# Kernel tuning notes

Measured on AMD Instinct MI355X. Metric: run time of the kernel, lower is better.

Reference implementation:

```python
import jax, jax.numpy as jnp
import numpy as np

S, P, T, E, H = 32, 48, 8, 64, 64      # scenes, peds/scene, obs_len, embedding_dim, h_dim
D1, D2 = 512, 1024                      # mlp_pre_pool hidden / bottleneck dims
B = S * P
TOTAL_LEN = 20                          # obs_len + pred_len (8 + 12)


def setup_inputs() -> dict:
    key = jax.random.key(0)
    ks = jax.random.split(key, 10)
    h_states = jax.random.normal(ks[0], (1, B, H), jnp.float32)
    end_pos = jax.random.normal(ks[1], (B, 2), jnp.float32)
    traj = jax.random.normal(ks[2], (TOTAL_LEN, B, 2), jnp.float32)
    traj_weight = jax.random.uniform(ks[3], (S, P * P, 2, T), jnp.float32)
    starts = jnp.arange(S, dtype=jnp.int32) * P
    seq_start_end = jnp.stack([starts, starts + P], axis=1)  # uniform scenes of P peds
    # learned params
    W_se = jax.random.normal(ks[4], (T * E, 2 * T), jnp.float32) * 0.05  # spatial_embedding
    b_se = jnp.zeros((T * E,), jnp.float32)
    W1 = jax.random.normal(ks[5], (D1, T * E + H), jnp.float32) * 0.05   # 576 -> 512
    b1 = jnp.zeros((D1,), jnp.float32)
    W2 = jax.random.normal(ks[6], (D2, D1), jnp.float32) * 0.05          # 512 -> 1024
    b2 = jnp.zeros((D2,), jnp.float32)
    return {"h_states": h_states, "seq_start_end": seq_start_end, "end_pos": end_pos,
            "traj": traj, "traj_weight": traj_weight, "mlp_pre_pool_dim_0": T * E,
            "W_se": W_se, "b_se": b_se, "W1": W1, "b1": b1, "W2": W2, "b2": b2}


def reference(h_states, seq_start_end, end_pos, traj, traj_weight, mlp_pre_pool_dim_0,
              W_se, b_se, W1, b1, W2, b2):
    # obs_traj: (obs_len, B, 2) -> (B, T, 2) -> per-scene (S, P, T, 2)
    obs = traj[:T].transpose(1, 0, 2).reshape(S, P, T, 2)
    h = h_states.reshape(S, P, H)
    # pairwise history differences: row (i, j) = obs[j] - obs[i]  (gather-diff)
    rel = obs[:, None, :, :, :] - obs[:, :, None, :, :]          # (S, i, j, T, 2)
    rel = rel.reshape(S, P, P, 2 * T)                            # flatten (T,2) -> 2T
    emb = rel @ W_se.T + b_se                                    # (S, P, P, T*E)
    # traj_weight[i]: (P*P, 2, T) -> permute(0,2,1) -> tile channel to E -> flatten
    w = jnp.transpose(traj_weight, (0, 1, 3, 2))                 # (S, P*P, T, 2)
    w = jnp.tile(w, (1, 1, 1, E // 2)).reshape(S, P, P, T * E)
    emb = w * emb
    # curr_hidden_1: hidden of ped j broadcast over i
    hj = jnp.broadcast_to(h[:, None, :, :], (S, P, P, H))
    x = jnp.concatenate([emb, hj], axis=-1)                      # (S, P, P, 576)
    x = jax.nn.relu(x @ W1.T + b1)                               # (S, P, P, 512)
    x = jax.nn.relu(x @ W2.T + b2)                               # (S, P, P, 1024)
    pool_h = x.max(axis=2)                                       # max over j
    return pool_h.reshape(S * P, D2)
```

## Files before the change

kernel.cpp:

```cpp
#include <hip/hip_runtime.h>
#include <hip/hip_bf16.h>
#include <stdint.h>

#define S_  32
#define P_  48
#define T_  8
#define E_  64
#define H_  64
#define D1_ 512
#define D2_ 1024
#define B_  (S_*P_)
#define M_  (S_*P_*P_)
#define K1_ 576
#define KE_ 512

typedef __attribute__((ext_vector_type(8))) short  short8;
typedef __attribute__((ext_vector_type(8))) __bf16 bf16x8;
typedef __attribute__((ext_vector_type(4))) float  f32x4;
typedef __attribute__((ext_vector_type(8))) float  f32x8;

__device__ inline short f2bf(float x) {
  union { float f; unsigned u; } v; v.f = x;
  unsigned r = v.u + 0x7FFFu + ((v.u >> 16) & 1u);
  return (short)(r >> 16);
}

__device__ inline void async16(const void* g, void* l) {
  __builtin_amdgcn_global_load_lds(
      (const __attribute__((address_space(1))) void*)g,
      (__attribute__((address_space(3))) void*)l, 16, 0, 0);
}

__device__ inline f32x4 mfma16(short8 a, short8 b, f32x4 c) {
  return __builtin_amdgcn_mfma_f32_16x16x32_bf16(
      __builtin_bit_cast(bf16x8, a), __builtin_bit_cast(bf16x8, b), c, 0, 0, 0);
}

#define LGKM0_FENCE() do { \
  asm volatile("s_waitcnt lgkmcnt(0)" ::: "memory"); \
  __builtin_amdgcn_sched_barrier(0); } while (0)

__global__ __launch_bounds__(256) void k_cvt_w(const float* __restrict__ W1,
                                               const float* __restrict__ W2,
                                               short* __restrict__ W1b,
                                               short* __restrict__ W2b) {
  int idx = blockIdx.x * 256 + threadIdx.x;
  if (idx < D1_ * K1_) W1b[idx] = f2bf(W1[idx]);
  int idx2 = idx - D1_ * K1_;
  if (idx2 >= 0 && idx2 < D2_ * D1_) W2b[idx2] = f2bf(W2[idx2]);
}

__global__ __launch_bounds__(256) void k_oW(const float* __restrict__ traj,
                                            const float* __restrict__ Wse,
                                            float* __restrict__ oW) {
  int bid = blockIdx.x;
  int p = bid >> 1;
  int n = ((bid & 1) << 8) + threadIdx.x;
  float obs[16];
#pragma unroll
  for (int t = 0; t < T_; ++t) {
    obs[2*t]   = traj[(t*B_ + p)*2 + 0];
    obs[2*t+1] = traj[(t*B_ + p)*2 + 1];
  }
  float acc = 0.f;
#pragma unroll
  for (int k = 0; k < 16; ++k) acc += obs[k] * Wse[n*16 + k];
  oW[p*KE_ + n] = acc;
}

__global__ __launch_bounds__(256) void k_build_x(const float* __restrict__ tw,
                                                 const float* __restrict__ h,
                                                 const float* __restrict__ bse,
                                                 const float* __restrict__ oW,
                                                 short* __restrict__ X) {
  int tid = threadIdx.x;
  int wid = tid >> 6, lane = tid & 63;
  int row = blockIdx.x * 4 + wid;
  int s   = row / (P_ * P_);
  int rem = row - s * (P_ * P_);
  int i   = rem / P_;
  int j   = rem - i * P_;
  int bi = s * P_ + i, bj = s * P_ + j;

  const float* twq = tw + (size_t)(s * (P_*P_) + rem) * 16;
  int t = lane >> 3;
  float w0 = twq[t];
  float w1 = twq[8 + t];

  int n0 = lane * 8;
  f32x8 vj = *(const f32x8*)&oW[(size_t)bj * KE_ + n0];
  f32x8 vi = *(const f32x8*)&oW[(size_t)bi * KE_ + n0];
  f32x8 vb = *(const f32x8*)&bse[n0];
  short8 o;
#pragma unroll
  for (int k = 0; k < 8; ++k) {
    float e = (vj[k] - vi[k] + vb[k]) * ((k & 1) ? w1 : w0);
    o[k] = f2bf(e);
  }
  *(short8*)&X[(size_t)row * K1_ + n0] = o;

  if (lane < 8) {
    f32x8 vh = *(const f32x8*)&h[(size_t)bj * H_ + lane * 8];
    short8 oh;
#pragma unroll
    for (int k = 0; k < 8; ++k) oh[k] = f2bf(vh[k]);
    *(short8*)&X[(size_t)row * K1_ + KE_ + lane * 8] = oh;
  }
}

__global__ __launch_bounds__(256, 2) void k_gemm1(const short* __restrict__ X,
                                                  const short* __restrict__ W1b,
                                                  const float* __restrict__ b1,
                                                  short* __restrict__ X1) {
  __shared__ short Abuf[2][128 * 64];
  __shared__ short Bbuf[2][128 * 64];
  int tid = threadIdx.x;
  int wid = tid >> 6, lane = tid & 63;
  int wgid = (blockIdx.x & 7) * 288 + (blockIdx.x >> 3);
  int tm = wgid >> 2, tn = wgid & 3;
  int brow = tm * 128, bcol = tn * 128;
  int wr = wid >> 1, wc = wid & 1;
  int lr = lane & 15, lhi = lane >> 4;
  int sx = lr & 7;

  f32x4 acc[4][4];
#pragma unroll
  for (int m = 0; m < 4; ++m)
#pragma unroll
    for (int n = 0; n < 4; ++n) acc[m][n] = (f32x4){0.f, 0.f, 0.f, 0.f};

  auto stageA = [&](int buf, int k0) {
#pragma unroll
    for (int it = 0; it < 4; ++it) {
      int fg = it * 256 + tid;
      int r = fg >> 3, gs = (fg & 7) ^ (r & 7);
      async16(&X[(size_t)(brow + r) * K1_ + k0 + (gs << 3)], &Abuf[buf][fg * 8]);
    }
  };
  auto stageB = [&](int buf, int k0) {
#pragma unroll
    for (int it = 0; it < 4; ++it) {
      int fg = it * 256 + tid;
      int r = fg >> 3, gs = (fg & 7) ^ (r & 7);
      async16(&W1b[(size_t)(bcol + r) * K1_ + k0 + (gs << 3)], &Bbuf[buf][fg * 8]);
    }
  };
  auto dsA = [&](int buf, int kk, short8* a) {
    int gr = kk * 4 + lhi;
#pragma unroll
    for (int m = 0; m < 4; ++m)
      a[m] = *(const short8*)&Abuf[buf][(wr*64 + m*16 + lr) * 64 + ((gr ^ sx) << 3)];
  };
  auto dsB = [&](int buf, int kk, short8* b) {
    int gr = kk * 4 + lhi;
#pragma unroll
    for (int n = 0; n < 4; ++n)
      b[n] = *(const short8*)&Bbuf[buf][(wc*64 + n*16 + lr) * 64 + ((gr ^ sx) << 3)];
  };
  auto mf16 = [&](short8* a, short8* b) {
    __builtin_amdgcn_s_setprio(1);
#pragma unroll
    for (int m = 0; m < 4; ++m)
#pragma unroll
      for (int n = 0; n < 4; ++n)
        acc[m][n] = mfma16(a[m], b[n], acc[m][n]);
    __builtin_amdgcn_s_setprio(0);
  };

  const int NT = 9;
  stageA(0, 0); stageB(0, 0);
  asm volatile("s_waitcnt vmcnt(0)" ::: "memory");
  __builtin_amdgcn_s_barrier();
#pragma unroll
  for (int t = 0; t < NT; ++t) {
    int bf = t & 1;
    short8 a0[4], b0[4];
    dsA(bf, 0, a0); dsB(bf, 0, b0);
    if (t + 1 < NT) stageA(bf ^ 1, (t + 1) * 64);
    __builtin_amdgcn_s_barrier();
    LGKM0_FENCE();
    mf16(a0, b0);
    __builtin_amdgcn_s_barrier();
    short8 a1[4], b1[4];
    dsA(bf, 1, a1); dsB(bf, 1, b1);
    if (t + 1 < NT) stageB(bf ^ 1, (t + 1) * 64);
    __builtin_amdgcn_s_barrier();
    LGKM0_FENCE();
    mf16(a1, b1);
    if (t + 1 < NT) {
      asm volatile("s_waitcnt vmcnt(0)" ::: "memory");
      __builtin_amdgcn_s_barrier();
    }
  }

#pragma unroll
  for (int n = 0; n < 4; ++n) {
    int gcol = bcol + wc*64 + n*16 + lr;
    float bias = b1[gcol];
#pragma unroll
    for (int m = 0; m < 4; ++m) {
      int grow0 = brow + wr*64 + m*16 + lhi*4;
#pragma unroll
      for (int q = 0; q < 4; ++q) {
        float v = acc[m][n][q] + bias;
        v = v > 0.f ? v : 0.f;
        X1[(size_t)(grow0 + q) * D1_ + gcol] = f2bf(v);
      }
    }
  }
}

__global__ __launch_bounds__(512, 2) void k_gemm2(const short* __restrict__ X1,
                                                  const short* __restrict__ W2b,
                                                  const float* __restrict__ b2,
                                                  float* __restrict__ out) {
  __shared__ short Abuf[2][192 * 64];
  __shared__ short Bbuf[3][256 * 64];
  int tid = threadIdx.x;
  int wid = tid >> 6, lane = tid & 63;
  int wgid = (blockIdx.x & 7) * 192 + (blockIdx.x >> 3);
  int tm = wgid >> 2, tn = wgid & 3;
  int brow = tm * 192, bcol = tn * 256;
  int wr = wid >> 2, wc = wid & 3;
  int lr = lane & 15, lhi = lane >> 4;
  int sx = lr & 7;

  f32x4 acc[6][4];
#pragma unroll
  for (int m = 0; m < 6; ++m)
#pragma unroll
    for (int n = 0; n < 4; ++n) acc[m][n] = (f32x4){0.f, 0.f, 0.f, 0.f};

  auto stageA = [&](int buf, int k0) {
#pragma unroll
    for (int it = 0; it < 3; ++it) {
      int fg = it * 512 + tid;
      int r = fg >> 3, gs = (fg & 7) ^ (r & 7);
      async16(&X1[(size_t)(brow + r) * D1_ + k0 + (gs << 3)], &Abuf[buf][fg * 8]);
    }
  };
  auto stageBh = [&](int buf, int k0, int half) {
#pragma unroll
    for (int it = 0; it < 2; ++it) {
      int fg = (half * 2 + it) * 512 + tid;
      int r = fg >> 3, gs = (fg & 7) ^ (r & 7);
      async16(&W2b[(size_t)(bcol + r) * D1_ + k0 + (gs << 3)], &Bbuf[buf][fg * 8]);
    }
  };
  auto dsA3 = [&](int buf, int kk, int mb, short8* a) {
    int gr = kk * 4 + lhi;
#pragma unroll
    for (int m = 0; m < 3; ++m)
      a[m] = *(const short8*)&Abuf[buf][(wr*96 + (mb + m)*16 + lr) * 64 + ((gr ^ sx) << 3)];
  };
  auto dsB4 = [&](int buf, int kk, short8* b) {
    int gr = kk * 4 + lhi;
#pragma unroll
    for (int n = 0; n < 4; ++n)
      b[n] = *(const short8*)&Bbuf[buf][(wc*64 + n*16 + lr) * 64 + ((gr ^ sx) << 3)];
  };
  auto mf12 = [&](short8* a, short8* b, int mb) {
    __builtin_amdgcn_s_setprio(1);
#pragma unroll
    for (int m = 0; m < 3; ++m)
#pragma unroll
      for (int n = 0; n < 4; ++n)
        acc[mb + m][n] = mfma16(a[m], b[n], acc[mb + m][n]);
    __builtin_amdgcn_s_setprio(0);
  };

  const int NT = 8;
  stageA(0, 0); stageBh(0, 0, 0); stageBh(0, 0, 1);
  stageBh(1, 64, 0); stageBh(1, 64, 1);
  asm volatile("s_waitcnt vmcnt(4)" ::: "memory");
  __builtin_amdgcn_s_barrier();
#pragma unroll
  for (int t = 0; t < NT; ++t) {
    int bA = t & 1, bB = t % 3;
    short8 a0[3], b0[4];
    dsA3(bA, 0, 0, a0); dsB4(bB, 0, b0);
    if (t + 1 < NT) stageA(bA ^ 1, (t + 1) * 64);
    __builtin_amdgcn_s_barrier();
    LGKM0_FENCE();
    mf12(a0, b0, 0);
    __builtin_amdgcn_s_barrier();
    short8 a1[3];
    dsA3(bA, 0, 3, a1);
    if (t + 2 < NT) stageBh((t + 2) % 3, (t + 2) * 64, 0);
    __builtin_amdgcn_s_barrier();
    LGKM0_FENCE();
    mf12(a1, b0, 3);
    __builtin_amdgcn_s_barrier();
    short8 a2[3], b1[4];
    dsA3(bA, 1, 0, a2); dsB4(bB, 1, b1);
    if (t + 2 < NT) stageBh((t + 2) % 3, (t + 2) * 64, 1);
    __builtin_amdgcn_s_barrier();
    LGKM0_FENCE();
    mf12(a2, b1, 0);
    __builtin_amdgcn_s_barrier();
    short8 a3[3];
    dsA3(bA, 1, 3, a3);
    __builtin_amdgcn_s_barrier();
    LGKM0_FENCE();
    mf12(a3, b1, 3);
    if (t + 2 < NT)      { asm volatile("s_waitcnt vmcnt(4)" ::: "memory"); }
    else if (t + 1 < NT) { asm volatile("s_waitcnt vmcnt(0)" ::: "memory"); }
    if (t + 1 < NT) __builtin_amdgcn_s_barrier();
  }

  int gbase = tm * 4 + wr * 2;
#pragma unroll
  for (int n = 0; n < 4; ++n) {
    int gcol = bcol + wc*64 + n*16 + lr;
    float bias = b2[gcol];
    float r0 = 0.f, r1 = 0.f;
#pragma unroll
    for (int m = 0; m < 3; ++m)
#pragma unroll
      for (int q = 0; q < 4; ++q) {
        float v0 = acc[m][n][q] + bias;
        float v1 = acc[m + 3][n][q] + bias;
        if (v0 > r0) r0 = v0;
        if (v1 > r1) r1 = v1;
      }
    r0 = fmaxf(r0, __shfl_xor(r0, 16));
    r0 = fmaxf(r0, __shfl_xor(r0, 32));
    r1 = fmaxf(r1, __shfl_xor(r1, 16));
    r1 = fmaxf(r1, __shfl_xor(r1, 32));
    if (lhi == 0) {
      out[(size_t)gbase       * D2_ + gcol] = r0;
      out[(size_t)(gbase + 1) * D2_ + gcol] = r1;
    }
  }
}

extern "C" void kernel_launch(void* const* d_in, const int* in_sizes, int n_in,
                              void* d_out, int out_size, void* d_ws, size_t ws_size,
                              hipStream_t stream) {
  const float* h_states = (const float*)d_in[0];
  const float* traj = (const float*)d_in[3];
  const float* tw   = (const float*)d_in[4];
  const float* Wse  = (const float*)d_in[6];
  const float* bse  = (const float*)d_in[7];
  const float* W1   = (const float*)d_in[8];
  const float* b1   = (const float*)d_in[9];
  const float* W2   = (const float*)d_in[10];
  const float* b2   = (const float*)d_in[11];
  float* out = (float*)d_out;

  char* ws = (char*)d_ws;
  const size_t X_BYTES   = (size_t)M_ * K1_ * 2;
  const size_t X1_BYTES  = (size_t)M_ * D1_ * 2;
  const size_t W1B_BYTES = (size_t)D1_ * K1_ * 2;
  short* X   = (short*)ws;
  short* X1  = (short*)(ws + X_BYTES);
  short* W1b = (short*)(ws + X_BYTES + X1_BYTES);
  short* W2b = (short*)(ws + X_BYTES + X1_BYTES + W1B_BYTES);
  float* oW  = (float*)(ws + X_BYTES);

  k_cvt_w  <<<(D1_*K1_ + D2_*D1_ + 255) / 256, 256, 0, stream>>>(W1, W2, W1b, W2b);
  k_oW     <<<B_ * 2, 256, 0, stream>>>(traj, Wse, oW);
  k_build_x<<<M_ / 4, 256, 0, stream>>>(tw, h_states, bse, oW, X);
  k_gemm1  <<<(M_ / 128) * (D1_ / 128), 256, 0, stream>>>(X, W1b, b1, X1);
  k_gemm2  <<<(M_ / 192) * (D2_ / 256), 512, 0, stream>>>(X1, W2b, b2, out);
}
```

Baseline: 248.1 us.

## Fuse pairwise embedding construction into first GEMM's A-tile staging

Removes the separate build_x kernel and its materialized bf16 X matrix (M x 576). The first GEMM now computes each A tile on the fly from oW, bias, traj_weight and h, writing it to LDS, and swaps the MFMA operand order so the epilogue writes vectorized 4-wide bf16 rows with a vector bias load. This saves a large global write and read of X, but replaces the async global-to-LDS loads with synchronous loads plus ALU work, and simplifies the pipeline to one barrier per K step. Each block recomputes rows that other column tiles also compute.

```diff
diff --git a/kernel.cpp b/kernel.cpp
--- a/kernel.cpp
+++ b/kernel.cpp
@@ -13,8 +13,10 @@
 #define M_  (S_*P_*P_)
 #define K1_ 576
 #define KE_ 512
+#define SPP 2304
 
 typedef __attribute__((ext_vector_type(8))) short  short8;
+typedef __attribute__((ext_vector_type(4))) short  short4v;
 typedef __attribute__((ext_vector_type(8))) __bf16 bf16x8;
 typedef __attribute__((ext_vector_type(4))) float  f32x4;
 typedef __attribute__((ext_vector_type(8))) float  f32x8;
@@ -68,50 +70,13 @@
   oW[p*KE_ + n] = acc;
 }
 
-__global__ __launch_bounds__(256) void k_build_x(const float* __restrict__ tw,
-                                                 const float* __restrict__ h,
-                                                 const float* __restrict__ bse,
-                                                 const float* __restrict__ oW,
-                                                 short* __restrict__ X) {
-  int tid = threadIdx.x;
-  int wid = tid >> 6, lane = tid & 63;
-  int row = blockIdx.x * 4 + wid;
-  int s   = row / (P_ * P_);
-  int rem = row - s * (P_ * P_);
-  int i   = rem / P_;
-  int j   = rem - i * P_;
-  int bi = s * P_ + i, bj = s * P_ + j;
-
-  const float* twq = tw + (size_t)(s * (P_*P_) + rem) * 16;
-  int t = lane >> 3;
-  float w0 = twq[t];
-  float w1 = twq[8 + t];
-
-  int n0 = lane * 8;
-  f32x8 vj = *(const f32x8*)&oW[(size_t)bj * KE_ + n0];
-  f32x8 vi = *(const f32x8*)&oW[(size_t)bi * KE_ + n0];
-  f32x8 vb = *(const f32x8*)&bse[n0];
-  short8 o;
-#pragma unroll
-  for (int k = 0; k < 8; ++k) {
-    float e = (vj[k] - vi[k] + vb[k]) * ((k & 1) ? w1 : w0);
-    o[k] = f2bf(e);
-  }
-  *(short8*)&X[(size_t)row * K1_ + n0] = o;
-
-  if (lane < 8) {
-    f32x8 vh = *(const f32x8*)&h[(size_t)bj * H_ + lane * 8];
-    short8 oh;
-#pragma unroll
-    for (int k = 0; k < 8; ++k) oh[k] = f2bf(vh[k]);
-    *(short8*)&X[(size_t)row * K1_ + KE_ + lane * 8] = oh;
-  }
-}
-
-__global__ __launch_bounds__(256, 2) void k_gemm1(const short* __restrict__ X,
-                                                  const short* __restrict__ W1b,
-                                                  const float* __restrict__ b1,
-                                                  short* __restrict__ X1) {
+__global__ __launch_bounds__(256, 2) void k_gemm1f(const float* __restrict__ oW,
+                                                   const float* __restrict__ bse,
+                                                   const float* __restrict__ tw,
+                                                   const float* __restrict__ h,
+                                                   const short* __restrict__ W1b,
+                                                   const float* __restrict__ b1,
+                                                   short* __restrict__ X1) {
   __shared__ short Abuf[2][128 * 64];
   __shared__ short Bbuf[2][128 * 64];
   int tid = threadIdx.x;
@@ -123,18 +88,46 @@
   int lr = lane & 15, lhi = lane >> 4;
   int sx = lr & 7;
 
+  int s     = brow / SPP;
+  int rem0  = brow - s * SPP;
+  int sbase = s * P_;
+  const float* tw16 = tw + (size_t)s * SPP * 16;
+
   f32x4 acc[4][4];
 #pragma unroll
   for (int m = 0; m < 4; ++m)
 #pragma unroll
     for (int n = 0; n < 4; ++n) acc[m][n] = (f32x4){0.f, 0.f, 0.f, 0.f};
 
-  auto stageA = [&](int buf, int k0) {
+  auto buildA = [&](int buf, int kt) {
+    int k0 = kt * 64;
 #pragma unroll
     for (int it = 0; it < 4; ++it) {
       int fg = it * 256 + tid;
       int r = fg >> 3, gs = (fg & 7) ^ (r & 7);
-      async16(&X[(size_t)(brow + r) * K1_ + k0 + (gs << 3)], &Abuf[buf][fg * 8]);
+      int rem_r = rem0 + r;
+      int jj = rem_r % P_;
+      int bj = sbase + jj;
+      short8 o;
+      if (kt < 8) {
+        int n0 = k0 + (gs << 3);
+        f32x8 vj = *(const f32x8*)&oW[(size_t)bj * KE_ + n0];
+        int ii = rem_r / P_;
+        f32x8 vi = *(const f32x8*)&oW[(size_t)(sbase + ii) * KE_ + n0];
+        f32x8 vb = *(const f32x8*)&bse[n0];
+        float w0 = tw16[rem_r * 16 + kt];
+        float w1 = tw16[rem_r * 16 + 8 + kt];
+#pragma unroll
+        for (int e = 0; e < 8; ++e) {
+          float v = (vj[e] - vi[e] + vb[e]) * ((e & 1) ? w1 : w0);
+          o[e] = f2bf(v);
+        }
+      } else {
+        f32x8 vh = *(const f32x8*)&h[(size_t)bj * H_ + (gs << 3)];
+#pragma unroll
+        for (int e = 0; e < 8; ++e) o[e] = f2bf(vh[e]);
+      }
+      *(short8*)&Abuf[buf][fg * 8] = o;
     }
   };
   auto stageB = [&](int buf, int k0) {
@@ -145,67 +138,56 @@
       async16(&W1b[(size_t)(bcol + r) * K1_ + k0 + (gs << 3)], &Bbuf[buf][fg * 8]);
     }
   };
-  auto dsA = [&](int buf, int kk, short8* a) {
-    int gr = kk * 4 + lhi;
-#pragma unroll
-    for (int m = 0; m < 4; ++m)
-      a[m] = *(const short8*)&Abuf[buf][(wr*64 + m*16 + lr) * 64 + ((gr ^ sx) << 3)];
-  };
-  auto dsB = [&](int buf, int kk, short8* b) {
-    int gr = kk * 4 + lhi;
-#pragma unroll
-    for (int n = 0; n < 4; ++n)
-      b[n] = *(const short8*)&Bbuf[buf][(wc*64 + n*16 + lr) * 64 + ((gr ^ sx) << 3)];
-  };
-  auto mf16 = [&](short8* a, short8* b) {
-    __builtin_amdgcn_s_setprio(1);
-#pragma unroll
-    for (int m = 0; m < 4; ++m)
+  auto compute = [&](int buf) {
+#pragma unroll
+    for (int kk = 0; kk < 2; ++kk) {
+      int gr = kk * 4 + lhi;
+      short8 a[4], b[4];
+#pragma unroll
+      for (int m = 0; m < 4; ++m)
+        a[m] = *(const short8*)&Abuf[buf][(wr*64 + m*16 + lr) * 64 + ((gr ^ sx) << 3)];
 #pragma unroll
       for (int n = 0; n < 4; ++n)
-        acc[m][n] = mfma16(a[m], b[n], acc[m][n]);
-    __builtin_amdgcn_s_setprio(0);
+        b[n] = *(const short8*)&Bbuf[buf][(wc*64 + n*16 + lr) * 64 + ((gr ^ sx) << 3)];
+      __builtin_amdgcn_s_setprio(1);
+#pragma unroll
+      for (int m = 0; m < 4; ++m)
+#pragma unroll
+        for (int n = 0; n < 4; ++n)
+          acc[m][n] = mfma16(b[n], a[m], acc[m][n]);
+      __builtin_amdgcn_s_setprio(0);
+    }
   };
 
   const int NT = 9;
-  stageA(0, 0); stageB(0, 0);
-  asm volatile("s_waitcnt vmcnt(0)" ::: "memory");
-  __builtin_amdgcn_s_barrier();
-#pragma unroll
+  stageB(0, 0);
+  buildA(0, 0);
+  __syncthreads();
   for (int t = 0; t < NT; ++t) {
     int bf = t & 1;
-    short8 a0[4], b0[4];
-    dsA(bf, 0, a0); dsB(bf, 0, b0);
-    if (t + 1 < NT) stageA(bf ^ 1, (t + 1) * 64);
-    __builtin_amdgcn_s_barrier();
-    LGKM0_FENCE();
-    mf16(a0, b0);
-    __builtin_amdgcn_s_barrier();
-    short8 a1[4], b1[4];
-    dsA(bf, 1, a1); dsB(bf, 1, b1);
-    if (t + 1 < NT) stageB(bf ^ 1, (t + 1) * 64);
-    __builtin_amdgcn_s_barrier();
-    LGKM0_FENCE();
-    mf16(a1, b1);
     if (t + 1 < NT) {
-      asm volatile("s_waitcnt vmcnt(0)" ::: "memory");
-      __builtin_amdgcn_s_barrier();
-    }
-  }
-
-#pragma unroll
-  for (int n = 0; n < 4; ++n) {
-    int gcol = bcol + wc*64 + n*16 + lr;
-    float bias = b1[gcol];
-#pragma unroll
-    for (int m = 0; m < 4; ++m) {
-      int grow0 = brow + wr*64 + m*16 + lhi*4;
+      stageB(bf ^ 1, (t + 1) * 64);
+      buildA(bf ^ 1, t + 1);
+    }
+    compute(bf);
+    __syncthreads();
+  }
+
+#pragma unroll
+  for (int m = 0; m < 4; ++m) {
+    int grow = brow + wr*64 + m*16 + lr;
+#pragma unroll
+    for (int n = 0; n < 4; ++n) {
+      int colbase = bcol + wc*64 + n*16 + lhi*4;
+      f32x4 bias = *(const f32x4*)&b1[colbase];
+      short4v o;
 #pragma unroll
       for (int q = 0; q < 4; ++q) {
-        float v = acc[m][n][q] + bias;
+        float v = acc[m][n][q] + bias[q];
         v = v > 0.f ? v : 0.f;
-        X1[(size_t)(grow0 + q) * D1_ + gcol] = f2bf(v);
+        o[q] = f2bf(v);
       }
+      *(short4v*)&X1[(size_t)grow * D1_ + colbase] = o;
     }
   }
 }
@@ -349,18 +331,17 @@
   float* out = (float*)d_out;
 
   char* ws = (char*)d_ws;
-  const size_t X_BYTES   = (size_t)M_ * K1_ * 2;
   const size_t X1_BYTES  = (size_t)M_ * D1_ * 2;
   const size_t W1B_BYTES = (size_t)D1_ * K1_ * 2;
-  short* X   = (short*)ws;
-  short* X1  = (short*)(ws + X_BYTES);
-  short* W1b = (short*)(ws + X_BYTES + X1_BYTES);
-  short* W2b = (short*)(ws + X_BYTES + X1_BYTES + W1B_BYTES);
-  float* oW  = (float*)(ws + X_BYTES);
-
-  k_cvt_w  <<<(D1_*K1_ + D2_*D1_ + 255) / 256, 256, 0, stream>>>(W1, W2, W1b, W2b);
-  k_oW     <<<B_ * 2, 256, 0, stream>>>(traj, Wse, oW);
-  k_build_x<<<M_ / 4, 256, 0, stream>>>(tw, h_states, bse, oW, X);
-  k_gemm1  <<<(M_ / 128) * (D1_ / 128), 256, 0, stream>>>(X, W1b, b1, X1);
-  k_gemm2  <<<(M_ / 192) * (D2_ / 256), 512, 0, stream>>>(X1, W2b, b2, out);
-}
+  const size_t W2B_BYTES = (size_t)D2_ * D1_ * 2;
+  short* X1  = (short*)ws;
+  short* W1b = (short*)(ws + X1_BYTES);
+  short* W2b = (short*)(ws + X1_BYTES + W1B_BYTES);
+  float* oW  = (float*)(ws + X1_BYTES + W1B_BYTES + W2B_BYTES);
+
+  k_cvt_w <<<(D1_*K1_ + D2_*D1_ + 255) / 256, 256, 0, stream>>>(W1, W2, W1b, W2b);
+  k_oW    <<<B_ * 2, 256, 0, stream>>>(traj, Wse, oW);
+  k_gemm1f<<<(M_ / 128) * (D1_ / 128), 256, 0, stream>>>(oW, bse, tw, h_states,
+                                                         W1b, b1, X1);
+  k_gemm2 <<<(M_ / 192) * (D2_ / 256), 512, 0, stream>>>(X1, W2b, b2, out);
+}
```

Result: slower. 280.4 us (+13.0%).
